# Optimization experiments

Hardware: AMD Instinct MI355X
Metric: run time of the kernel (lower is better)

## Reference

```python
import jax, jax.numpy as jnp
import numpy as np

E = 1024   # embed_dim
H = 16     # num_heads
D = E // H # head_dim
M = 2048   # query length
N = 2048   # key/value length
B = 4      # batch
SCALE = 1.0 / float(np.sqrt(D))


def setup_inputs() -> dict:
    key = jax.random.key(0)
    ks = jax.random.split(key, 11)
    s = 0.02
    return {
        "query": jax.random.normal(ks[0], (M, B, E), jnp.float32),
        "key": jax.random.normal(ks[1], (N, B, E), jnp.float32),
        "value": jax.random.normal(ks[2], (N, B, E), jnp.float32),
        "Wq": jax.random.normal(ks[3], (E, E), jnp.float32) * s,
        "bq": jax.random.normal(ks[4], (E,), jnp.float32) * s,
        "Wk": jax.random.normal(ks[5], (E, E), jnp.float32) * s,
        "bk": jax.random.normal(ks[6], (E,), jnp.float32) * s,
        "Wv": jax.random.normal(ks[7], (E, E), jnp.float32) * s,
        "bv": jax.random.normal(ks[8], (E,), jnp.float32) * s,
        "Wo": jax.random.normal(ks[9], (E, E), jnp.float32) * s,
        "bo": jax.random.normal(ks[10], (E,), jnp.float32) * s,
    }


def reference(query, key, value, Wq, bq, Wk, bk, Wv, bv, Wo, bo):
    # batch_first=False: (M,B,E) -> (B,M,E)
    q = jnp.swapaxes(query, 0, 1)
    k = jnp.swapaxes(key, 0, 1)
    v = jnp.swapaxes(value, 0, 1)
    # projections (torch Linear: x @ W^T + b; here W stored as (in,out))
    q = (q @ Wq + bq).reshape(B, M, H, D)
    k = (k @ Wk + bk).reshape(B, N, H, D)
    v = (v @ Wv + bv).reshape(B, N, H, D)
    # per-head attention, vectorized over heads (same math as the Python loop)
    logits = jnp.einsum("bmhd,bnhd->bhmn", q, k) * SCALE
    attn = jax.nn.softmax(logits, axis=-1)
    out = jnp.einsum("bhmn,bnhd->bmhd", attn, v).reshape(B, M, E)
    out = out @ Wo + bo
    # back to (M,B,E)
    return jnp.swapaxes(out, 0, 1)
```

## Files before the change

### kernel.cpp

```cpp
#include <hip/hip_runtime.h>

typedef unsigned short u16;
typedef __bf16 bf16x8 __attribute__((ext_vector_type(8)));
typedef float f32x4 __attribute__((ext_vector_type(4)));
typedef unsigned short u16x8 __attribute__((ext_vector_type(8)));
typedef unsigned short u16x4 __attribute__((ext_vector_type(4)));

#define LOG2E 1.44269504088896f

__device__ __forceinline__ float fast_exp2(float x) {
#if __has_builtin(__builtin_amdgcn_exp2f)
  return __builtin_amdgcn_exp2f(x);
#else
  return exp2f(x);
#endif
}

__device__ __forceinline__ u16 f2bf(float x) {
  union { __bf16 b; u16 u; } c;
  c.b = (__bf16)x;
  return c.u;
}

__device__ __forceinline__ void gload_lds16(const void* g, void* l) {
  __builtin_amdgcn_global_load_lds(
      (__attribute__((address_space(1))) void*)(g),
      (__attribute__((address_space(3))) void*)(l), 16, 0, 0);
}

__device__ __forceinline__ int swz_off(int row, int col) {
  return row * 64 + ((((col >> 3) ^ (row ^ (row >> 3))) & 7) << 3) + (col & 7);
}

__global__ __launch_bounds__(256) void transpose_cvt4(
    const float* __restrict__ Wq, const float* __restrict__ Wk,
    const float* __restrict__ Wv, const float* __restrict__ Wo,
    u16* __restrict__ Wqt, u16* __restrict__ Wkt,
    u16* __restrict__ Wvt, u16* __restrict__ Wot) {
  const int E = 1024;
  const float* W = blockIdx.z == 0 ? Wq : blockIdx.z == 1 ? Wk
                   : blockIdx.z == 2 ? Wv : Wo;
  u16* Wt = blockIdx.z == 0 ? Wqt : blockIdx.z == 1 ? Wkt
            : blockIdx.z == 2 ? Wvt : Wot;
  __shared__ float tile[32][33];
  int tx = threadIdx.x & 31, ty = threadIdx.x >> 5;
  int bx = blockIdx.x * 32, by = blockIdx.y * 32;
  #pragma unroll
  for (int i = 0; i < 32; i += 8)
    tile[ty + i][tx] = W[(size_t)(by + ty + i) * E + bx + tx];
  __syncthreads();
  #pragma unroll
  for (int i = 0; i < 32; i += 8)
    Wt[(size_t)(bx + ty + i) * E + by + tx] = f2bf(tile[tx][ty + i]);
}

__global__ __launch_bounds__(256) void proj_qkv(
    const float* __restrict__ Xq, const float* __restrict__ Xk,
    const float* __restrict__ Xv,
    const u16* __restrict__ Wqt, const u16* __restrict__ Wkt,
    const u16* __restrict__ Wvt,
    const float* __restrict__ bq, const float* __restrict__ bk,
    const float* __restrict__ bv,
    u16* __restrict__ Qp, u16* __restrict__ Kp, u16* __restrict__ Vp,
    float qscale)
{
  constexpr int K = 1024, N = 1024;
  const float* A; const u16* Bt; const float* bias; u16* C; float oscale;
  if (blockIdx.z == 0)      { A = Xq; Bt = Wqt; bias = bq; C = Qp; oscale = qscale; }
  else if (blockIdx.z == 1) { A = Xk; Bt = Wkt; bias = bk; C = Kp; oscale = 1.f; }
  else                      { A = Xv; Bt = Wvt; bias = bv; C = Vp; oscale = 1.f; }

  __shared__ u16 As[128 * 64];
  __shared__ u16 Bs[128 * 64];
  const int tid = threadIdx.x;
  const int w = tid >> 6;
  const int lane = tid & 63;
  const int lo = lane & 15, hi = lane >> 4;
  const int brow = blockIdx.x * 128;
  const int bcol = blockIdx.y * 128;
  const int wr = (w >> 1) * 64;
  const int wc = (w & 1) * 64;

  f32x4 acc[4][4] = {};

  for (int k0 = 0; k0 < K; k0 += 64) {
    __syncthreads();
    #pragma unroll
    for (int i = 0; i < 4; i++) {
      int c = i * 256 + tid;
      int rowo = c >> 3;
      int ko = (c & 7) * 8;
      gload_lds16(Bt + (size_t)(bcol + rowo) * K + k0 + ko,
                  (void*)(Bs + (size_t)(i * 256 + w * 64) * 8));
    }
    #pragma unroll
    for (int i = 0; i < 4; i++) {
      int c = i * 256 + tid;
      int rowo = c >> 3;
      int ko = (c & 7) * 8;
      const float* Ap = A + (size_t)(brow + rowo) * K + k0 + ko;
      float4 v0 = *(const float4*)Ap;
      float4 v1 = *(const float4*)(Ap + 4);
      u16x8 ab;
      ab[0] = f2bf(v0.x); ab[1] = f2bf(v0.y); ab[2] = f2bf(v0.z); ab[3] = f2bf(v0.w);
      ab[4] = f2bf(v1.x); ab[5] = f2bf(v1.y); ab[6] = f2bf(v1.z); ab[7] = f2bf(v1.w);
      *(u16x8*)(As + swz_off(rowo, ko)) = ab;
    }
    __syncthreads();
    #pragma unroll
    for (int kk = 0; kk < 2; kk++) {
      bf16x8 af[4], bfr[4];
      #pragma unroll
      for (int mi = 0; mi < 4; mi++)
        af[mi] = *(const bf16x8*)(As + swz_off(wr + mi * 16 + lo, kk * 32 + hi * 8));
      #pragma unroll
      for (int ni = 0; ni < 4; ni++)
        bfr[ni] = *(const bf16x8*)(Bs + (wc + ni * 16 + lo) * 64 + kk * 32 + hi * 8);
      #pragma unroll
      for (int mi = 0; mi < 4; mi++)
        #pragma unroll
        for (int ni = 0; ni < 4; ni++)
          acc[mi][ni] = __builtin_amdgcn_mfma_f32_16x16x32_bf16(
              af[mi], bfr[ni], acc[mi][ni], 0, 0, 0);
    }
  }

  #pragma unroll
  for (int mi = 0; mi < 4; mi++)
    #pragma unroll
    for (int ni = 0; ni < 4; ni++) {
      int row = brow + wr + mi * 16 + hi * 4;
      int col = bcol + wc + ni * 16 + lo;
      float bv = bias[col];
      #pragma unroll
      for (int r = 0; r < 4; r++) {
        float v = (acc[mi][ni][r] + bv) * oscale;
        C[(size_t)(row + r) * N + col] = f2bf(v);
      }
    }
}

__global__ __launch_bounds__(256) void gemm_out(
    const u16* __restrict__ A, const u16* __restrict__ Bt,
    const float* __restrict__ bias, float* __restrict__ C)
{
  constexpr int K = 1024, N = 1024;
  __shared__ u16 As[128 * 64];
  __shared__ u16 Bs[128 * 64];
  const int tid = threadIdx.x;
  const int w = tid >> 6;
  const int lane = tid & 63;
  const int lo = lane & 15, hi = lane >> 4;
  const int brow = blockIdx.x * 128;
  const int bcol = blockIdx.y * 128;
  const int wr = (w >> 1) * 64;
  const int wc = (w & 1) * 64;

  f32x4 acc[4][4] = {};

  for (int k0 = 0; k0 < K; k0 += 64) {
    __syncthreads();
    #pragma unroll
    for (int i = 0; i < 4; i++) {
      int c = i * 256 + tid;
      int rowo = c >> 3;
      int ko = (c & 7) * 8;
      gload_lds16(A + (size_t)(brow + rowo) * K + k0 + ko,
                  (void*)(As + (size_t)(i * 256 + w * 64) * 8));
      gload_lds16(Bt + (size_t)(bcol + rowo) * K + k0 + ko,
                  (void*)(Bs + (size_t)(i * 256 + w * 64) * 8));
    }
    __syncthreads();
    #pragma unroll
    for (int kk = 0; kk < 2; kk++) {
      bf16x8 af[4], bfr[4];
      #pragma unroll
      for (int mi = 0; mi < 4; mi++)
        af[mi] = *(const bf16x8*)(As + (wr + mi * 16 + lo) * 64 + kk * 32 + hi * 8);
      #pragma unroll
      for (int ni = 0; ni < 4; ni++)
        bfr[ni] = *(const bf16x8*)(Bs + (wc + ni * 16 + lo) * 64 + kk * 32 + hi * 8);
      #pragma unroll
      for (int mi = 0; mi < 4; mi++)
        #pragma unroll
        for (int ni = 0; ni < 4; ni++)
          acc[mi][ni] = __builtin_amdgcn_mfma_f32_16x16x32_bf16(
              af[mi], bfr[ni], acc[mi][ni], 0, 0, 0);
    }
  }

  #pragma unroll
  for (int mi = 0; mi < 4; mi++)
    #pragma unroll
    for (int ni = 0; ni < 4; ni++) {
      int row = brow + wr + mi * 16 + hi * 4;
      int col = bcol + wc + ni * 16 + lo;
      float bv = bias[col];
      #pragma unroll
      for (int r = 0; r < 4; r++)
        C[(size_t)(row + r) * N + col] = acc[mi][ni][r] + bv;
    }
}

__global__ __launch_bounds__(256) void attn_kernel(
    const u16* __restrict__ Qp, const u16* __restrict__ Kp,
    const u16* __restrict__ Vp, u16* __restrict__ O)
{
  constexpr int Bb = 4, E = 1024, Nn = 2048, Dh = 64;
  constexpr float THR = 8.0f;
  __shared__ u16 Ks[2][64 * 64];
  __shared__ u16 Vt[2][64 * 64];
  __shared__ u16 Ps[4][32 * 64];

  const int tid = threadIdx.x;
  const int lane = tid & 63;
  const int w = tid >> 6;
  const int lo = lane & 15, hi = lane >> 4;

  const int wg = blockIdx.x;
  const int swz = (wg & 7) * 128 + (wg >> 3);
  const int b_ = swz >> 8;
  const int h = (swz >> 4) & 15;
  const int mbase = (swz & 15) * 128 + w * 32;

  bf16x8 q[2][2];
  #pragma unroll
  for (int mi = 0; mi < 2; mi++)
    #pragma unroll
    for (int kk = 0; kk < 2; kk++) {
      int m = mbase + mi * 16 + lo;
      q[mi][kk] = *(const bf16x8*)(Qp + (size_t)(m * Bb + b_) * E + h * Dh + kk * 32 + hi * 8);
    }

  f32x4 acc[2][4] = {};
  float mrun[2] = {-3e38f, -3e38f};
  float lrun[2] = {0.f, 0.f};

  const int nrK = tid >> 3;
  const int q8K = (tid & 7) * 8;
  const int dq = (tid & 15) * 4;
  const int nq = (tid >> 4) * 4;

  u16x8 kreg[2];
  u16x4 vreg[4];
  #pragma unroll
  for (int i = 0; i < 2; i++)
    kreg[i] = *(const u16x8*)(Kp + (size_t)((i * 32 + nrK) * Bb + b_) * E + h * Dh + q8K);
  #pragma unroll
  for (int j = 0; j < 4; j++)
    vreg[j] = *(const u16x4*)(Vp + (size_t)((nq + j) * Bb + b_) * E + h * Dh + dq);

  int it = 0;
  for (int n0 = 0; n0 < Nn; n0 += 64, it ^= 1) {
    #pragma unroll
    for (int i = 0; i < 2; i++)
      *(u16x8*)(&Ks[it][swz_off(i * 32 + nrK, q8K)]) = kreg[i];
    #pragma unroll
    for (int jw = 0; jw < 4; jw++) {
      u16x4 colv;
      #pragma unroll
      for (int j = 0; j < 4; j++) colv[j] = vreg[j][jw];
      *(u16x4*)(&Vt[it][swz_off(dq + jw, nq)]) = colv;
    }
    __syncthreads();
    if (n0 + 64 < Nn) {
      #pragma unroll
      for (int i = 0; i < 2; i++)
        kreg[i] = *(const u16x8*)(Kp + (size_t)((n0 + 64 + i * 32 + nrK) * Bb + b_) * E + h * Dh + q8K);
      #pragma unroll
      for (int j = 0; j < 4; j++)
        vreg[j] = *(const u16x4*)(Vp + (size_t)((n0 + 64 + nq + j) * Bb + b_) * E + h * Dh + dq);
    }
    const u16* ksp = &Ks[it][0];
    const u16* vtp = &Vt[it][0];

    f32x4 s[2][4];
    __builtin_amdgcn_s_setprio(1);
    #pragma unroll
    for (int ni = 0; ni < 4; ni++) {
      bf16x8 kf0 = *(const bf16x8*)(ksp + swz_off(ni * 16 + lo, hi * 8));
      bf16x8 kf1 = *(const bf16x8*)(ksp + swz_off(ni * 16 + lo, 32 + hi * 8));
      #pragma unroll
      for (int mi = 0; mi < 2; mi++) {
        f32x4 t = {};
        t = __builtin_amdgcn_mfma_f32_16x16x32_bf16(kf0, q[mi][0], t, 0, 0, 0);
        t = __builtin_amdgcn_mfma_f32_16x16x32_bf16(kf1, q[mi][1], t, 0, 0, 0);
        s[mi][ni] = t;
      }
    }
    __builtin_amdgcn_s_setprio(0);

    #pragma unroll
    for (int mi = 0; mi < 2; mi++) {
      f32x4 mx4 = s[mi][0];
      #pragma unroll
      for (int ni = 1; ni < 4; ni++) {
        #pragma unroll
        for (int r = 0; r < 4; r++) mx4[r] = fmaxf(mx4[r], s[mi][ni][r]);
      }
      float tm = fmaxf(fmaxf(mx4[0], mx4[1]), fmaxf(mx4[2], mx4[3]));
      if (!__all(tm <= mrun[mi] + THR)) {
        float g = fmaxf(tm, __shfl_xor(tm, 16));
        g = fmaxf(g, __shfl_xor(g, 32));
        float mn = fmaxf(mrun[mi], g);
        float al = fast_exp2(mrun[mi] - mn);
        mrun[mi] = mn;
        lrun[mi] *= al;
        #pragma unroll
        for (int df = 0; df < 4; df++) acc[mi][df] *= al;
      }
      const float m_ = mrun[mi];
      f32x4 rv = {0.f, 0.f, 0.f, 0.f};
      #pragma unroll
      for (int ni = 0; ni < 4; ni++) {
        #pragma unroll
        for (int r = 0; r < 4; r++) {
          float p = fast_exp2(s[mi][ni][r] - m_);
          s[mi][ni][r] = p;
          rv[r] += p;
        }
      }
      lrun[mi] += (rv[0] + rv[1]) + (rv[2] + rv[3]);
      #pragma unroll
      for (int ni = 0; ni < 4; ni++) {
        u16x4 pk;
        #pragma unroll
        for (int r = 0; r < 4; r++) pk[r] = f2bf(s[mi][ni][r]);
        *(u16x4*)(Ps[w] + swz_off(mi * 16 + lo, ni * 16 + hi * 4)) = pk;
      }
    }

    __builtin_amdgcn_s_setprio(1);
    #pragma unroll
    for (int kk = 0; kk < 2; kk++) {
      bf16x8 pf[2];
      #pragma unroll
      for (int mi = 0; mi < 2; mi++)
        pf[mi] = *(const bf16x8*)(Ps[w] + swz_off(mi * 16 + lo, kk * 32 + hi * 8));
      #pragma unroll
      for (int df = 0; df < 4; df++) {
        bf16x8 vf = *(const bf16x8*)(vtp + swz_off(df * 16 + lo, kk * 32 + hi * 8));
        #pragma unroll
        for (int mi = 0; mi < 2; mi++)
          acc[mi][df] = __builtin_amdgcn_mfma_f32_16x16x32_bf16(vf, pf[mi], acc[mi][df], 0, 0, 0);
      }
    }
    __builtin_amdgcn_s_setprio(0);
  }

  #pragma unroll
  for (int mi = 0; mi < 2; mi++) {
    float l = lrun[mi];
    l += __shfl_xor(l, 16);
    l += __shfl_xor(l, 32);
    float inv = 1.f / l;
    int m = mbase + mi * 16 + lo;
    #pragma unroll
    for (int df = 0; df < 4; df++) {
      u16x4 o;
      #pragma unroll
      for (int r = 0; r < 4; r++) o[r] = f2bf(acc[mi][df][r] * inv);
      *(u16x4*)(O + (size_t)(m * Bb + b_) * E + h * Dh + df * 16 + hi * 4) = o;
    }
  }
}

extern "C" void kernel_launch(void* const* d_in, const int* in_sizes, int n_in,
                              void* d_out, int out_size, void* d_ws, size_t ws_size,
                              hipStream_t stream) {
  const float* query = (const float*)d_in[0];
  const float* key   = (const float*)d_in[1];
  const float* value = (const float*)d_in[2];
  const float* Wq = (const float*)d_in[3];
  const float* bq = (const float*)d_in[4];
  const float* Wk = (const float*)d_in[5];
  const float* bk = (const float*)d_in[6];
  const float* Wv = (const float*)d_in[7];
  const float* bv = (const float*)d_in[8];
  const float* Wo = (const float*)d_in[9];
  const float* bo = (const float*)d_in[10];
  float* out = (float*)d_out;

  const float QSCALE = 0.125f * LOG2E;

  const size_t XE = (size_t)2048 * 4 * 1024;
  const size_t WE = (size_t)1024 * 1024;
  u16* ws  = (u16*)d_ws;
  u16* Qp  = ws;
  u16* Kp  = Qp + XE;
  u16* Vp  = Kp + XE;
  u16* Ob  = Vp + XE;
  u16* Wqt = Ob + XE;
  u16* Wkt = Wqt + WE;
  u16* Wvt = Wkt + WE;
  u16* Wot = Wvt + WE;

  dim3 blk(256);
  transpose_cvt4<<<dim3(32, 32, 4), blk, 0, stream>>>(
      Wq, Wk, Wv, Wo, Wqt, Wkt, Wvt, Wot);

  proj_qkv<<<dim3(64, 8, 3), blk, 0, stream>>>(
      query, key, value, Wqt, Wkt, Wvt, bq, bk, bv, Qp, Kp, Vp, QSCALE);

  attn_kernel<<<1024, blk, 0, stream>>>(Qp, Kp, Vp, Ob);

  gemm_out<<<dim3(64, 8), blk, 0, stream>>>(Ob, Wot, bo, out);
}
```

Measured before the change: 236.8 us.

## Switch attention to 32x32x16 MFMA and keep P in registers via permlane swap

Rewrites the attention inner loop to use 32x32x16 bf16 MFMA tiles instead of 16x16x32, so each lane owns a single query row and the softmax statistics become per-lane scalars. The P tile is converted to bf16 and rearranged into the B-operand layout with v_permlane32_swap instead of being written to and read back from a per-wave LDS buffer. This removes the P LDS round trip and cuts cross-lane reductions, but depends on the permlane layout mapping being exactly right and may raise register pressure.

```diff
diff --git a/kernel.cpp b/kernel.cpp
--- a/kernel.cpp
+++ b/kernel.cpp
@@ -1,8 +1,10 @@
 #include <hip/hip_runtime.h>
 
 typedef unsigned short u16;
+typedef unsigned int u32;
 typedef __bf16 bf16x8 __attribute__((ext_vector_type(8)));
 typedef float f32x4 __attribute__((ext_vector_type(4)));
+typedef float f32x16 __attribute__((ext_vector_type(16)));
 typedef unsigned short u16x8 __attribute__((ext_vector_type(8)));
 typedef unsigned short u16x4 __attribute__((ext_vector_type(4)));
 
@@ -20,6 +22,10 @@
   union { __bf16 b; u16 u; } c;
   c.b = (__bf16)x;
   return c.u;
+}
+
+__device__ __forceinline__ void permswap32(u32& a, u32& b) {
+  asm volatile("v_permlane32_swap_b32 %0, %1" : "+v"(a), "+v"(b));
 }
 
 __device__ __forceinline__ void gload_lds16(const void* g, void* l) {
@@ -206,35 +212,35 @@
     const u16* __restrict__ Qp, const u16* __restrict__ Kp,
     const u16* __restrict__ Vp, u16* __restrict__ O)
 {
-  constexpr int Bb = 4, E = 1024, Nn = 2048, Dh = 64;
+  constexpr int Bb = 4, E = 1024, Nn = 2048;
   constexpr float THR = 8.0f;
   __shared__ u16 Ks[2][64 * 64];
   __shared__ u16 Vt[2][64 * 64];
-  __shared__ u16 Ps[4][32 * 64];
 
   const int tid = threadIdx.x;
   const int lane = tid & 63;
   const int w = tid >> 6;
-  const int lo = lane & 15, hi = lane >> 4;
+  const int l31 = lane & 31;
+  const int hi5 = lane >> 5;
 
   const int wg = blockIdx.x;
   const int swz = (wg & 7) * 128 + (wg >> 3);
   const int b_ = swz >> 8;
   const int h = (swz >> 4) & 15;
   const int mbase = (swz & 15) * 128 + w * 32;
-
-  bf16x8 q[2][2];
-  #pragma unroll
-  for (int mi = 0; mi < 2; mi++)
-    #pragma unroll
-    for (int kk = 0; kk < 2; kk++) {
-      int m = mbase + mi * 16 + lo;
-      q[mi][kk] = *(const bf16x8*)(Qp + (size_t)(m * Bb + b_) * E + h * Dh + kk * 32 + hi * 8);
-    }
-
-  f32x4 acc[2][4] = {};
-  float mrun[2] = {-3e38f, -3e38f};
-  float lrun[2] = {0.f, 0.f};
+  const int m = mbase + l31;
+
+  bf16x8 q[4];
+  {
+    const u16* qrow = Qp + (size_t)(m * Bb + b_) * E + h * 64;
+    #pragma unroll
+    for (int kb = 0; kb < 4; kb++)
+      q[kb] = *(const bf16x8*)(qrow + kb * 16 + hi5 * 8);
+  }
+
+  f32x16 oacc[2] = {};
+  float mrun = -3e38f;
+  float lrun = 0.f;
 
   const int nrK = tid >> 3;
   const int q8K = (tid & 7) * 8;
@@ -245,10 +251,10 @@
   u16x4 vreg[4];
   #pragma unroll
   for (int i = 0; i < 2; i++)
-    kreg[i] = *(const u16x8*)(Kp + (size_t)((i * 32 + nrK) * Bb + b_) * E + h * Dh + q8K);
+    kreg[i] = *(const u16x8*)(Kp + (size_t)((i * 32 + nrK) * Bb + b_) * E + h * 64 + q8K);
   #pragma unroll
   for (int j = 0; j < 4; j++)
-    vreg[j] = *(const u16x4*)(Vp + (size_t)((nq + j) * Bb + b_) * E + h * Dh + dq);
+    vreg[j] = *(const u16x4*)(Vp + (size_t)((nq + j) * Bb + b_) * E + h * 64 + dq);
 
   int it = 0;
   for (int n0 = 0; n0 < Nn; n0 += 64, it ^= 1) {
@@ -266,101 +272,97 @@
     if (n0 + 64 < Nn) {
       #pragma unroll
       for (int i = 0; i < 2; i++)
-        kreg[i] = *(const u16x8*)(Kp + (size_t)((n0 + 64 + i * 32 + nrK) * Bb + b_) * E + h * Dh + q8K);
+        kreg[i] = *(const u16x8*)(Kp + (size_t)((n0 + 64 + i * 32 + nrK) * Bb + b_) * E + h * 64 + q8K);
       #pragma unroll
       for (int j = 0; j < 4; j++)
-        vreg[j] = *(const u16x4*)(Vp + (size_t)((n0 + 64 + nq + j) * Bb + b_) * E + h * Dh + dq);
+        vreg[j] = *(const u16x4*)(Vp + (size_t)((n0 + 64 + nq + j) * Bb + b_) * E + h * 64 + dq);
     }
     const u16* ksp = &Ks[it][0];
     const u16* vtp = &Vt[it][0];
 
-    f32x4 s[2][4];
+    f32x16 st[2];
     __builtin_amdgcn_s_setprio(1);
     #pragma unroll
-    for (int ni = 0; ni < 4; ni++) {
-      bf16x8 kf0 = *(const bf16x8*)(ksp + swz_off(ni * 16 + lo, hi * 8));
-      bf16x8 kf1 = *(const bf16x8*)(ksp + swz_off(ni * 16 + lo, 32 + hi * 8));
-      #pragma unroll
-      for (int mi = 0; mi < 2; mi++) {
-        f32x4 t = {};
-        t = __builtin_amdgcn_mfma_f32_16x16x32_bf16(kf0, q[mi][0], t, 0, 0, 0);
-        t = __builtin_amdgcn_mfma_f32_16x16x32_bf16(kf1, q[mi][1], t, 0, 0, 0);
-        s[mi][ni] = t;
+    for (int sb = 0; sb < 2; sb++) {
+      f32x16 t = {};
+      #pragma unroll
+      for (int kb = 0; kb < 4; kb++) {
+        bf16x8 kf = *(const bf16x8*)(ksp + swz_off(sb * 32 + l31, kb * 16 + hi5 * 8));
+        t = __builtin_amdgcn_mfma_f32_32x32x16_bf16(kf, q[kb], t, 0, 0, 0);
       }
+      st[sb] = t;
     }
     __builtin_amdgcn_s_setprio(0);
 
-    #pragma unroll
-    for (int mi = 0; mi < 2; mi++) {
-      f32x4 mx4 = s[mi][0];
-      #pragma unroll
-      for (int ni = 1; ni < 4; ni++) {
-        #pragma unroll
-        for (int r = 0; r < 4; r++) mx4[r] = fmaxf(mx4[r], s[mi][ni][r]);
+    float v16[16];
+    #pragma unroll
+    for (int i = 0; i < 16; i++) v16[i] = fmaxf(st[0][i], st[1][i]);
+    #pragma unroll
+    for (int i = 0; i < 8; i++) v16[i] = fmaxf(v16[i], v16[i + 8]);
+    #pragma unroll
+    for (int i = 0; i < 4; i++) v16[i] = fmaxf(v16[i], v16[i + 4]);
+    float tm = fmaxf(fmaxf(v16[0], v16[1]), fmaxf(v16[2], v16[3]));
+    if (!__all(tm <= mrun + THR)) {
+      float g = fmaxf(tm, __shfl_xor(tm, 32));
+      float mn = fmaxf(mrun, g);
+      float al = fast_exp2(mrun - mn);
+      mrun = mn;
+      lrun *= al;
+      oacc[0] *= al;
+      oacc[1] *= al;
+    }
+    const float m_ = mrun;
+
+    u32 pk[2][8];
+    float r0 = 0.f, r1 = 0.f, r2 = 0.f, r3 = 0.f;
+    #pragma unroll
+    for (int sb = 0; sb < 2; sb++) {
+      #pragma unroll
+      for (int j = 0; j < 8; j++) {
+        float p0 = fast_exp2(st[sb][2 * j] - m_);
+        float p1 = fast_exp2(st[sb][2 * j + 1] - m_);
+        if (j & 1) { r0 += p0; r1 += p1; } else { r2 += p0; r3 += p1; }
+        pk[sb][j] = (u32)f2bf(p0) | ((u32)f2bf(p1) << 16);
       }
-      float tm = fmaxf(fmaxf(mx4[0], mx4[1]), fmaxf(mx4[2], mx4[3]));
-      if (!__all(tm <= mrun[mi] + THR)) {
-        float g = fmaxf(tm, __shfl_xor(tm, 16));
-        g = fmaxf(g, __shfl_xor(g, 32));
-        float mn = fmaxf(mrun[mi], g);
-        float al = fast_exp2(mrun[mi] - mn);
-        mrun[mi] = mn;
-        lrun[mi] *= al;
-        #pragma unroll
-        for (int df = 0; df < 4; df++) acc[mi][df] *= al;
-      }
-      const float m_ = mrun[mi];
-      f32x4 rv = {0.f, 0.f, 0.f, 0.f};
-      #pragma unroll
-      for (int ni = 0; ni < 4; ni++) {
-        #pragma unroll
-        for (int r = 0; r < 4; r++) {
-          float p = fast_exp2(s[mi][ni][r] - m_);
-          s[mi][ni][r] = p;
-          rv[r] += p;
-        }
-      }
-      lrun[mi] += (rv[0] + rv[1]) + (rv[2] + rv[3]);
-      #pragma unroll
-      for (int ni = 0; ni < 4; ni++) {
-        u16x4 pk;
-        #pragma unroll
-        for (int r = 0; r < 4; r++) pk[r] = f2bf(s[mi][ni][r]);
-        *(u16x4*)(Ps[w] + swz_off(mi * 16 + lo, ni * 16 + hi * 4)) = pk;
-      }
+    }
+    lrun += (r0 + r1) + (r2 + r3);
+
+    bf16x8 pb[4];
+    #pragma unroll
+    for (int kb = 0; kb < 4; kb++) {
+      int sb = kb >> 1, c = kb & 1;
+      u32 a0 = pk[sb][4 * c + 0], b0 = pk[sb][4 * c + 2];
+      u32 a1 = pk[sb][4 * c + 1], b1 = pk[sb][4 * c + 3];
+      permswap32(a0, b0);
+      permswap32(a1, b1);
+      union { u32 d[4]; bf16x8 v; } u;
+      u.d[0] = a0; u.d[1] = a1; u.d[2] = b0; u.d[3] = b1;
+      pb[kb] = u.v;
     }
 
     __builtin_amdgcn_s_setprio(1);
     #pragma unroll
-    for (int kk = 0; kk < 2; kk++) {
-      bf16x8 pf[2];
-      #pragma unroll
-      for (int mi = 0; mi < 2; mi++)
-        pf[mi] = *(const bf16x8*)(Ps[w] + swz_off(mi * 16 + lo, kk * 32 + hi * 8));
-      #pragma unroll
-      for (int df = 0; df < 4; df++) {
-        bf16x8 vf = *(const bf16x8*)(vtp + swz_off(df * 16 + lo, kk * 32 + hi * 8));
-        #pragma unroll
-        for (int mi = 0; mi < 2; mi++)
-          acc[mi][df] = __builtin_amdgcn_mfma_f32_16x16x32_bf16(vf, pf[mi], acc[mi][df], 0, 0, 0);
+    for (int dsb = 0; dsb < 2; dsb++) {
+      #pragma unroll
+      for (int kb = 0; kb < 4; kb++) {
+        bf16x8 vf = *(const bf16x8*)(vtp + swz_off(dsb * 32 + l31, kb * 16 + hi5 * 8));
+        oacc[dsb] = __builtin_amdgcn_mfma_f32_32x32x16_bf16(vf, pb[kb], oacc[dsb], 0, 0, 0);
       }
     }
     __builtin_amdgcn_s_setprio(0);
   }
 
-  #pragma unroll
-  for (int mi = 0; mi < 2; mi++) {
-    float l = lrun[mi];
-    l += __shfl_xor(l, 16);
-    l += __shfl_xor(l, 32);
-    float inv = 1.f / l;
-    int m = mbase + mi * 16 + lo;
-    #pragma unroll
-    for (int df = 0; df < 4; df++) {
+  float l = lrun + __shfl_xor(lrun, 32);
+  float inv = 1.f / l;
+  u16* orow = O + (size_t)(m * Bb + b_) * E + h * 64;
+  #pragma unroll
+  for (int dsb = 0; dsb < 2; dsb++) {
+    #pragma unroll
+    for (int qd = 0; qd < 4; qd++) {
       u16x4 o;
       #pragma unroll
-      for (int r = 0; r < 4; r++) o[r] = f2bf(acc[mi][df][r] * inv);
-      *(u16x4*)(O + (size_t)(m * Bb + b_) * E + h * Dh + df * 16 + hi * 4) = o;
+      for (int t = 0; t < 4; t++) o[t] = f2bf(oacc[dsb][qd * 4 + t] * inv);
+      *(u16x4*)(orow + dsb * 32 + qd * 8 + hi5 * 4) = o;
     }
   }
 }
```

New measurement: 253.7 us. 7.1% more time.
